# Performance work log

Hardware: AMD Instinct MI355X
Metric: run time of the kernel (lower is better)

## Reference

```python
import jax, jax.numpy as jnp
import numpy as np

S = 4096      # total packed tokens
B = 8         # number of variable-length segments
E = 1152      # embed_dim (SigLIP2 so400m)
H = 16        # num_heads
D = E // H    # head_dim = 72


def setup_inputs() -> dict:
    key = jax.random.key(0)
    ks = jax.random.split(key, 8)
    w_std = 0.02
    theta = jax.random.uniform(ks[1], (S, D), jnp.float32, 0.0, 2.0 * np.pi)
    return {
        "hidden_states": jax.random.normal(ks[0], (S, E), jnp.float32),
        "cu_seqlens": jnp.arange(B + 1, dtype=jnp.int32) * (S // B),
        "cos": jnp.cos(theta),
        "sin": jnp.sin(theta),
        "Wq": jax.random.normal(ks[2], (E, E), jnp.float32) * w_std,
        "bq": jnp.zeros((E,), jnp.float32),
        "Wk": jax.random.normal(ks[3], (E, E), jnp.float32) * w_std,
        "bk": jnp.zeros((E,), jnp.float32),
        "Wv": jax.random.normal(ks[4], (E, E), jnp.float32) * w_std,
        "bv": jnp.zeros((E,), jnp.float32),
        "Wo": jax.random.normal(ks[5], (E, E), jnp.float32) * w_std,
        "bo": jnp.zeros((E,), jnp.float32),
    }


def _rotate_half(x):
    x1, x2 = jnp.split(x, 2, axis=-1)
    return jnp.concatenate((-x2, x1), axis=-1)


def reference(hidden_states, cu_seqlens, cos, sin, Wq, bq, Wk, bk, Wv, bv, Wo, bo):
    seq_len = hidden_states.shape[0]
    scale = np.float32(D) ** -0.5
    # projections -> [S, H, D]
    q = (hidden_states @ Wq.T + bq).reshape(seq_len, H, D)
    k = (hidden_states @ Wk.T + bk).reshape(seq_len, H, D)
    v = (hidden_states @ Wv.T + bv).reshape(seq_len, H, D)
    # inline RoPE (apply_rotary_pos_emb_vision): cos/sin broadcast over heads
    c = cos[:, None, :]
    s = sin[:, None, :]
    q = q * c + _rotate_half(q) * s
    k = k * c + _rotate_half(k) * s
    # segment id per token from cu_seqlens; block-diagonal attention mask
    seg = jnp.searchsorted(cu_seqlens[1:], jnp.arange(seq_len, dtype=cu_seqlens.dtype), side="right")
    mask = seg[:, None] == seg[None, :]                     # [S, S]
    scores = jnp.einsum("shd,thd->hst", q, k) * scale       # [H, S, S]
    neg = jnp.finfo(scores.dtype).min
    scores = jnp.where(mask[None, :, :], scores, neg)
    probs = jax.nn.softmax(scores, axis=-1)
    attn = jnp.einsum("hst,thd->shd", probs, v).reshape(seq_len, E)
    return attn @ Wo.T + bo
```

## Files before the change

### kernel.cpp

```cpp
#include <hip/hip_runtime.h>
#include <float.h>

#define S_LEN 4096
#define E_DIM 1152
#define NH    16
#define HD    72
#define HD2   36
#define NQKV  3456

typedef __attribute__((ext_vector_type(4))) float f32x4;
typedef __attribute__((ext_vector_type(8))) _Float16 f16x8;

__device__ __forceinline__ unsigned short f2h(float f) {
    union { _Float16 h; unsigned short u; } c;
    c.h = (_Float16)f;
    return c.u;
}

__device__ __forceinline__ void gload_lds16(const unsigned short* g, unsigned short* l) {
    __builtin_amdgcn_global_load_lds(
        (const __attribute__((address_space(1))) unsigned int*)g,
        (__attribute__((address_space(3))) unsigned int*)l, 16, 0, 0);
}

__global__ __launch_bounds__(256)
void pack_f16(const float* __restrict__ hs, const float* __restrict__ wq,
              const float* __restrict__ wk, const float* __restrict__ wv,
              const float* __restrict__ wo,
              unsigned short* __restrict__ hs_h, unsigned short* __restrict__ wqkv_h,
              unsigned short* __restrict__ wo_h)
{
    const float* src; unsigned short* dst; int n4;
    const int WSZ = E_DIM * E_DIM;
    switch (blockIdx.z) {
        case 0: src = hs; dst = hs_h;             n4 = S_LEN * E_DIM / 4; break;
        case 1: src = wq; dst = wqkv_h;           n4 = WSZ / 4; break;
        case 2: src = wk; dst = wqkv_h + WSZ;     n4 = WSZ / 4; break;
        case 3: src = wv; dst = wqkv_h + 2 * WSZ; n4 = WSZ / 4; break;
        default: src = wo; dst = wo_h;            n4 = WSZ / 4; break;
    }
    for (int i = blockIdx.x * 256 + threadIdx.x; i < n4; i += gridDim.x * 256) {
        f32x4 x = ((const f32x4*)src)[i];
        ushort4 hv;
        hv.x = f2h(x[0]); hv.y = f2h(x[1]); hv.z = f2h(x[2]); hv.w = f2h(x[3]);
        ((ushort4*)dst)[i] = hv;
    }
}

__global__ __launch_bounds__(256, 4)
void gemm_qkv_f16(const unsigned short* __restrict__ Ah, const unsigned short* __restrict__ Wh,
                  const float* __restrict__ bq, const float* __restrict__ bk,
                  const float* __restrict__ bv,
                  float* __restrict__ oq, float* __restrict__ ok, float* __restrict__ ov)
{
    __shared__ unsigned short sA[128 * 64];
    __shared__ unsigned short sB[128 * 64];
    const int tid  = threadIdx.x;
    const int w    = tid >> 6, lane = tid & 63;
    const int quad = lane >> 4, m = lane & 15;
    const int wr   = w & 1,  wc = w >> 1;

    const int bid = blockIdx.x;
    const int lin = (bid & 7) * 108 + (bid >> 3);
    const int n_t = lin >> 5;
    const int m_t = lin & 31;
    const int m0  = m_t * 128;
    const int n0  = n_t * 128;

    const int srow = lane >> 3;
    const int skc  = (lane & 7) ^ srow;

    f32x4 acc[4][4];
    #pragma unroll
    for (int i = 0; i < 4; ++i)
        #pragma unroll
        for (int j = 0; j < 4; ++j) acc[i][j] = (f32x4){0.f, 0.f, 0.f, 0.f};

    const int rm7 = m & 7;

    for (int k0 = 0; k0 < E_DIM; k0 += 64) {
        #pragma unroll
        for (int c = 0; c < 4; ++c) {
            int r = 32 * w + 8 * c + srow;
            gload_lds16(Ah + (size_t)(m0 + r) * E_DIM + k0 + skc * 8, &sA[(32 * w + 8 * c) * 64]);
            gload_lds16(Wh + (size_t)(n0 + r) * E_DIM + k0 + skc * 8, &sB[(32 * w + 8 * c) * 64]);
        }
        __syncthreads();

        #pragma unroll
        for (int k3 = 0; k3 < 2; ++k3) {
            f16x8 ah[4], bh[4];
            #pragma unroll
            for (int t = 0; t < 4; ++t) {
                int pc = ((k3 << 2) + quad) ^ rm7;
                ah[t] = *(const f16x8*)&sA[(64 * wr + 16 * t + m) * 64 + pc * 8];
                bh[t] = *(const f16x8*)&sB[(64 * wc + 16 * t + m) * 64 + pc * 8];
            }
            #pragma unroll
            for (int rt = 0; rt < 4; ++rt)
                #pragma unroll
                for (int ct = 0; ct < 4; ++ct)
                    acc[rt][ct] = __builtin_amdgcn_mfma_f32_16x16x32_f16(ah[rt], bh[ct], acc[rt][ct], 0, 0, 0);
        }
        __syncthreads();
    }

    const int which = n0 / E_DIM;
    const int n0l = n0 - which * E_DIM;
    const float* bp = (which == 0) ? bq : (which == 1) ? bk : bv;
    float* Cp       = (which == 0) ? oq : (which == 1) ? ok : ov;
    #pragma unroll
    for (int ct = 0; ct < 4; ++ct) {
        int col = n0l + 64 * wc + 16 * ct + m;
        float bias = bp[col];
        #pragma unroll
        for (int rt = 0; rt < 4; ++rt)
            #pragma unroll
            for (int reg = 0; reg < 4; ++reg) {
                int row = m0 + 64 * wr + 16 * rt + 4 * quad + reg;
                Cp[(size_t)row * E_DIM + col] = acc[rt][ct][reg] + bias;
            }
    }
}

__global__ __launch_bounds__(256, 4)
void gemm_out_f16(const unsigned short* __restrict__ Ah, const unsigned short* __restrict__ Wh,
                  const float* __restrict__ bo, float* __restrict__ Cp)
{
    __shared__ unsigned short sA[64 * 64];
    __shared__ unsigned short sB[128 * 64];
    const int tid  = threadIdx.x;
    const int w    = tid >> 6, lane = tid & 63;
    const int quad = lane >> 4, m = lane & 15;
    const int m0   = blockIdx.y * 64;
    const int n0   = blockIdx.x * 128;

    const int srow = lane >> 3;
    const int skc  = (lane & 7) ^ srow;

    f32x4 acc[4][2];
    #pragma unroll
    for (int i = 0; i < 4; ++i)
        #pragma unroll
        for (int j = 0; j < 2; ++j) acc[i][j] = (f32x4){0.f, 0.f, 0.f, 0.f};

    const int rm7 = m & 7;

    for (int k0 = 0; k0 < E_DIM; k0 += 64) {
        #pragma unroll
        for (int c = 0; c < 2; ++c) {
            int r = 16 * w + 8 * c + srow;
            gload_lds16(Ah + (size_t)(m0 + r) * E_DIM + k0 + skc * 8, &sA[(16 * w + 8 * c) * 64]);
        }
        #pragma unroll
        for (int c = 0; c < 4; ++c) {
            int r = 32 * w + 8 * c + srow;
            gload_lds16(Wh + (size_t)(n0 + r) * E_DIM + k0 + skc * 8, &sB[(32 * w + 8 * c) * 64]);
        }
        __syncthreads();
        #pragma unroll
        for (int k3 = 0; k3 < 2; ++k3) {
            f16x8 ah[4], bh[2];
            int pc = ((k3 << 2) + quad) ^ rm7;
            #pragma unroll
            for (int t = 0; t < 4; ++t)
                ah[t] = *(const f16x8*)&sA[(16 * t + m) * 64 + pc * 8];
            #pragma unroll
            for (int ct = 0; ct < 2; ++ct)
                bh[ct] = *(const f16x8*)&sB[(32 * w + 16 * ct + m) * 64 + pc * 8];
            #pragma unroll
            for (int rt = 0; rt < 4; ++rt)
                #pragma unroll
                for (int ct = 0; ct < 2; ++ct)
                    acc[rt][ct] = __builtin_amdgcn_mfma_f32_16x16x32_f16(ah[rt], bh[ct], acc[rt][ct], 0, 0, 0);
        }
        __syncthreads();
    }

    #pragma unroll
    for (int ct = 0; ct < 2; ++ct) {
        int col = n0 + 32 * w + 16 * ct + m;
        float bias = bo[col];
        #pragma unroll
        for (int rt = 0; rt < 4; ++rt)
            #pragma unroll
            for (int reg = 0; reg < 4; ++reg) {
                int row = m0 + 16 * rt + 4 * quad + reg;
                Cp[(size_t)row * E_DIM + col] = acc[rt][ct][reg] + bias;
            }
    }
}

__global__ __launch_bounds__(256)
void vtrans(const float* __restrict__ v, unsigned short* __restrict__ vt)
{
    __shared__ unsigned short tile[HD][72];
    const int h = blockIdx.y;
    const int s0 = blockIdx.x * 64;
    for (int task = threadIdx.x; task < 64 * 18; task += 256) {
        int r = task / 18, c = task % 18;
        f32x4 x = *(const f32x4*)(v + (size_t)(s0 + r) * E_DIM + h * HD + (c << 2));
        tile[(c << 2) + 0][r] = f2h(x[0]);
        tile[(c << 2) + 1][r] = f2h(x[1]);
        tile[(c << 2) + 2][r] = f2h(x[2]);
        tile[(c << 2) + 3][r] = f2h(x[3]);
    }
    __syncthreads();
    for (int task = threadIdx.x; task < HD * 8; task += 256) {
        int d = task / 8, cc = task % 8;
        uint4 val = *(const uint4*)&tile[d][cc << 3];
        *(uint4*)(vt + ((size_t)h * HD + d) * S_LEN + s0 + (cc << 3)) = val;
    }
}

__global__ __launch_bounds__(256, 4)
void attn_rope(const float* __restrict__ qf, const float* __restrict__ kf,
               const float* __restrict__ cosb, const float* __restrict__ sinb,
               const unsigned short* __restrict__ vt, const int* __restrict__ cu,
               int nseg, unsigned short* __restrict__ out)
{
    __shared__ unsigned short ks_s[64][72];
    __shared__ unsigned short vs_s[80][72];
    __shared__ unsigned short ss_s[64][72];

    const int tid  = threadIdx.x;
    const int w    = tid >> 6;
    const int lane = tid & 63;
    const int quad = lane >> 4;
    const int m    = lane & 15;
    const int h    = blockIdx.y;
    const int qb0  = blockIdx.x * 64;
    const float scale = 0.11785113019775793f;

    {
        uint4 zz = make_uint4(0u, 0u, 0u, 0u);
        if (tid < 72) {
            int r = 72 + tid / 9, c = tid % 9;
            *(uint4*)&vs_s[r][c << 3] = zz;
        }
    }

    int rs_r[4], re_r[4];
    #pragma unroll
    for (int reg = 0; reg < 4; ++reg) {
        int row = qb0 + 16 * w + 4 * quad + reg;
        int st = 0;
        for (int i = 1; i < nseg; ++i) if (cu[i] <= row) st = i;
        rs_r[reg] = cu[st];
        re_r[reg] = cu[st + 1];
    }
    int st0 = 0, st1 = 0;
    for (int i = 1; i < nseg; ++i) {
        if (cu[i] <= qb0) st0 = i;
        if (cu[i] <= qb0 + 63) st1 = i;
    }
    const int kstart = cu[st0];
    const int kend   = cu[st1 + 1];

    for (int task = tid; task < 64 * 9; task += 256) {
        int row = task / 9, d0 = (task % 9) << 2;
        int s = qb0 + row;
        const float* xr = qf + (size_t)s * E_DIM + h * HD;
        f32x4 a  = *(const f32x4*)(xr + d0);
        f32x4 b  = *(const f32x4*)(xr + d0 + HD2);
        f32x4 c1 = *(const f32x4*)(cosb + (size_t)s * HD + d0);
        f32x4 s1 = *(const f32x4*)(sinb + (size_t)s * HD + d0);
        f32x4 c2 = *(const f32x4*)(cosb + (size_t)s * HD + d0 + HD2);
        f32x4 s2 = *(const f32x4*)(sinb + (size_t)s * HD + d0 + HD2);
        f32x4 r1 = a * c1 - b * s1;
        f32x4 r2 = b * c2 + a * s2;
        uint2 u1, u2;
        u1.x = (unsigned)f2h(r1[0]) | ((unsigned)f2h(r1[1]) << 16);
        u1.y = (unsigned)f2h(r1[2]) | ((unsigned)f2h(r1[3]) << 16);
        u2.x = (unsigned)f2h(r2[0]) | ((unsigned)f2h(r2[1]) << 16);
        u2.y = (unsigned)f2h(r2[2]) | ((unsigned)f2h(r2[3]) << 16);
        *(uint2*)&ks_s[row][d0]       = u1;
        *(uint2*)&ks_s[row][d0 + HD2] = u2;
    }
    __syncthreads();

    f16x8 qfr[3];
    {
        const unsigned short* qrow = &ks_s[16 * w + m][0];
        #pragma unroll
        for (int k3 = 0; k3 < 3; ++k3) {
            bool pad = (k3 == 2) && (quad != 0);
            int off = pad ? 0 : (k3 * 32 + quad * 8);
            f16x8 val = *(const f16x8*)(qrow + off);
            f16x8 z = {0, 0, 0, 0, 0, 0, 0, 0};
            qfr[k3] = pad ? z : val;
        }
    }

    f32x4 acc_o[5];
    #pragma unroll
    for (int i = 0; i < 5; ++i) acc_o[i] = (f32x4){0.f, 0.f, 0.f, 0.f};
    float l_r[4] = {0.f, 0.f, 0.f, 0.f};

    for (int kb_i = kstart; kb_i < kend; kb_i += 64) {
        __syncthreads();
        for (int task = tid; task < 64 * 9; task += 256) {
            int row = task / 9, d0 = (task % 9) << 2;
            int s = kb_i + row; if (s >= kend) s = kend - 1;
            const float* xr = kf + (size_t)s * E_DIM + h * HD;
            f32x4 a  = *(const f32x4*)(xr + d0);
            f32x4 b  = *(const f32x4*)(xr + d0 + HD2);
            f32x4 c1 = *(const f32x4*)(cosb + (size_t)s * HD + d0);
            f32x4 s1 = *(const f32x4*)(sinb + (size_t)s * HD + d0);
            f32x4 c2 = *(const f32x4*)(cosb + (size_t)s * HD + d0 + HD2);
            f32x4 s2 = *(const f32x4*)(sinb + (size_t)s * HD + d0 + HD2);
            f32x4 r1 = a * c1 - b * s1;
            f32x4 r2 = b * c2 + a * s2;
            uint2 u1, u2;
            u1.x = (unsigned)f2h(r1[0]) | ((unsigned)f2h(r1[1]) << 16);
            u1.y = (unsigned)f2h(r1[2]) | ((unsigned)f2h(r1[3]) << 16);
            u2.x = (unsigned)f2h(r2[0]) | ((unsigned)f2h(r2[1]) << 16);
            u2.y = (unsigned)f2h(r2[2]) | ((unsigned)f2h(r2[3]) << 16);
            *(uint2*)&ks_s[row][d0]       = u1;
            *(uint2*)&ks_s[row][d0 + HD2] = u2;
        }
        for (int slot = tid; slot < 72 * 8; slot += 256) {
            int d = slot / 8, c = slot % 8;
            int kk0 = kb_i + (c << 3);
            if (kk0 > S_LEN - 8) kk0 = S_LEN - 8;
            uint4 val = *(const uint4*)(vt + ((size_t)h * HD + d) * S_LEN + kk0);
            *(uint4*)&vs_s[d][c << 3] = val;
        }
        __syncthreads();

        f32x4 sacc[4];
        #pragma unroll
        for (int ct = 0; ct < 4; ++ct) sacc[ct] = (f32x4){0.f, 0.f, 0.f, 0.f};
        #pragma unroll
        for (int ct = 0; ct < 4; ++ct) {
            const unsigned short* krow = &ks_s[16 * ct + m][0];
            #pragma unroll
            for (int k3 = 0; k3 < 3; ++k3) {
                bool pad = (k3 == 2) && (quad != 0);
                int off = pad ? 0 : (k3 * 32 + quad * 8);
                f16x8 bfr = *(const f16x8*)(krow + off);
                f16x8 z = {0, 0, 0, 0, 0, 0, 0, 0};
                bfr = pad ? z : bfr;
                sacc[ct] = __builtin_amdgcn_mfma_f32_16x16x32_f16(qfr[k3], bfr, sacc[ct], 0, 0, 0);
            }
        }

        #pragma unroll
        for (int ct = 0; ct < 4; ++ct) {
            int key = kb_i + 16 * ct + m;
            #pragma unroll
            for (int reg = 0; reg < 4; ++reg) {
                bool valid = (key >= rs_r[reg]) && (key < re_r[reg]);
                float p = valid ? __expf(sacc[ct][reg] * scale) : 0.f;
                l_r[reg] += p;
                ss_s[16 * w + 4 * quad + reg][16 * ct + m] = f2h(p);
            }
        }

        {
            const unsigned short* prow = &ss_s[16 * w + m][0];
            f16x8 pf0 = *(const f16x8*)(prow + quad * 8);
            f16x8 pf1 = *(const f16x8*)(prow + 32 + quad * 8);
            #pragma unroll
            for (int ct2 = 0; ct2 < 5; ++ct2) {
                const unsigned short* vrow = &vs_s[16 * ct2 + m][0];
                f16x8 vf0 = *(const f16x8*)(vrow + quad * 8);
                f16x8 vf1 = *(const f16x8*)(vrow + 32 + quad * 8);
                acc_o[ct2] = __builtin_amdgcn_mfma_f32_16x16x32_f16(pf0, vf0, acc_o[ct2], 0, 0, 0);
                acc_o[ct2] = __builtin_amdgcn_mfma_f32_16x16x32_f16(pf1, vf1, acc_o[ct2], 0, 0, 0);
            }
        }
    }

    #pragma unroll
    for (int reg = 0; reg < 4; ++reg) {
        float l = l_r[reg];
        l += __shfl_xor(l, 1);
        l += __shfl_xor(l, 2);
        l += __shfl_xor(l, 4);
        l += __shfl_xor(l, 8);
        l_r[reg] = l;
    }

    #pragma unroll
    for (int reg = 0; reg < 4; ++reg) {
        float linv = (l_r[reg] > 0.f) ? 1.f / l_r[reg] : 0.f;
        int row = qb0 + 16 * w + 4 * quad + reg;
        unsigned short* orow = out + (size_t)row * E_DIM + h * HD;
        #pragma unroll
        for (int ct2 = 0; ct2 < 5; ++ct2) {
            int col = 16 * ct2 + m;
            if (col < HD) orow[col] = f2h(acc_o[ct2][reg] * linv);
        }
    }
}

extern "C" void kernel_launch(void* const* d_in, const int* in_sizes, int n_in,
                              void* d_out, int out_size, void* d_ws, size_t ws_size,
                              hipStream_t stream)
{
    const float* hs   = (const float*)d_in[0];
    const int*   cu   = (const int*)d_in[1];
    const float* cosb = (const float*)d_in[2];
    const float* sinb = (const float*)d_in[3];
    const float* Wq   = (const float*)d_in[4];
    const float* bq   = (const float*)d_in[5];
    const float* Wk   = (const float*)d_in[6];
    const float* bk   = (const float*)d_in[7];
    const float* Wv   = (const float*)d_in[8];
    const float* bv   = (const float*)d_in[9];
    const float* Wo   = (const float*)d_in[10];
    const float* bo   = (const float*)d_in[11];
    float* outp = (float*)d_out;

    const size_t mat = (size_t)S_LEN * E_DIM;
    float* qf = (float*)d_ws;
    float* kf = qf + mat;
    float* vf = kf + mat;
    unsigned short* hs_h   = (unsigned short*)(vf + mat);
    unsigned short* wqkv_h = hs_h + mat;
    unsigned short* wo_h   = wqkv_h + (size_t)NQKV * E_DIM;
    unsigned short* vtb    = wo_h + (size_t)E_DIM * E_DIM;
    unsigned short* attn_h = hs_h;

    const int nseg = in_sizes[1] - 1;

    dim3 gpack(512, 1, 5);
    pack_f16<<<gpack, 256, 0, stream>>>(hs, Wq, Wk, Wv, Wo, hs_h, wqkv_h, wo_h);

    gemm_qkv_f16<<<dim3(864), 256, 0, stream>>>(hs_h, wqkv_h, bq, bk, bv, qf, kf, vf);

    dim3 gvt(S_LEN / 64, NH, 1);
    vtrans<<<gvt, 256, 0, stream>>>(vf, vtb);

    dim3 gattn(S_LEN / 64, NH, 1);
    attn_rope<<<gattn, 256, 0, stream>>>(qf, kf, cosb, sinb, vtb, cu, nseg, attn_h);

    dim3 gout(E_DIM / 128, S_LEN / 64, 1);
    gemm_out_f16<<<gout, 256, 0, stream>>>(attn_h, wo_h, bo, outp);
}
```

Measured before the change: 224.3 us.

## Precompute RoPE'd fp16 Q/K and pass attention probabilities via register shuffles

RoPE and the fp16 conversion of Q and K move out of the attention loop into a pre-pass kernel that also transposes V. This stops each query block from recomputing RoPE on every K tile. The attention kernel now loads head-major fp16 K directly and computes S^T so the probabilities can be rearranged into the P·V operand with lane shuffles instead of an LDS round-trip. Packed conversion intrinsics replace scalar f16 conversions. The cost is extra global traffic for the fp16 Q/K buffers and one more read pass over q/k in the pre-pass kernel.

```diff
diff --git a/kernel.cpp b/kernel.cpp
--- a/kernel.cpp
+++ b/kernel.cpp
@@ -9,11 +9,17 @@
 #define NQKV  3456
 
 typedef __attribute__((ext_vector_type(4))) float f32x4;
+typedef __attribute__((ext_vector_type(2))) __fp16 fp16v2;
 typedef __attribute__((ext_vector_type(8))) _Float16 f16x8;
 
 __device__ __forceinline__ unsigned short f2h(float f) {
     union { _Float16 h; unsigned short u; } c;
     c.h = (_Float16)f;
+    return c.u;
+}
+__device__ __forceinline__ unsigned pack2h(float a, float b) {
+    union { fp16v2 v; unsigned u; } c;
+    c.v = __builtin_amdgcn_cvt_pkrtz(a, b);
     return c.u;
 }
 
@@ -41,9 +47,10 @@
     }
     for (int i = blockIdx.x * 256 + threadIdx.x; i < n4; i += gridDim.x * 256) {
         f32x4 x = ((const f32x4*)src)[i];
-        ushort4 hv;
-        hv.x = f2h(x[0]); hv.y = f2h(x[1]); hv.z = f2h(x[2]); hv.w = f2h(x[3]);
-        ((ushort4*)dst)[i] = hv;
+        uint2 hv;
+        hv.x = pack2h(x[0], x[1]);
+        hv.y = pack2h(x[2], x[3]);
+        ((uint2*)dst)[i] = hv;
     }
 }
 
@@ -192,36 +199,64 @@
 }
 
 __global__ __launch_bounds__(256)
-void vtrans(const float* __restrict__ v, unsigned short* __restrict__ vt)
+void rope_v_pack(const float* __restrict__ qf, const float* __restrict__ kf,
+                 const float* __restrict__ vf,
+                 const float* __restrict__ cosb, const float* __restrict__ sinb,
+                 unsigned short* __restrict__ qb, unsigned short* __restrict__ kb,
+                 unsigned short* __restrict__ vt)
 {
     __shared__ unsigned short tile[HD][72];
-    const int h = blockIdx.y;
+    const int h  = blockIdx.y;
     const int s0 = blockIdx.x * 64;
-    for (int task = threadIdx.x; task < 64 * 18; task += 256) {
-        int r = task / 18, c = task % 18;
-        f32x4 x = *(const f32x4*)(v + (size_t)(s0 + r) * E_DIM + h * HD + (c << 2));
-        tile[(c << 2) + 0][r] = f2h(x[0]);
-        tile[(c << 2) + 1][r] = f2h(x[1]);
-        tile[(c << 2) + 2][r] = f2h(x[2]);
-        tile[(c << 2) + 3][r] = f2h(x[3]);
-    }
-    __syncthreads();
-    for (int task = threadIdx.x; task < HD * 8; task += 256) {
-        int d = task / 8, cc = task % 8;
-        uint4 val = *(const uint4*)&tile[d][cc << 3];
-        *(uint4*)(vt + ((size_t)h * HD + d) * S_LEN + s0 + (cc << 3)) = val;
+    const int z  = blockIdx.z;
+    if (z < 2) {
+        const float* x = (z == 0) ? qf : kf;
+        unsigned short* ob = (z == 0) ? qb : kb;
+        for (int task = threadIdx.x; task < 64 * 9; task += 256) {
+            int sl = task / 9, c = task % 9;
+            int s = s0 + sl;
+            int d0 = c << 2;
+            const float* xr = x + (size_t)s * E_DIM + h * HD;
+            f32x4 a  = *(const f32x4*)(xr + d0);
+            f32x4 b  = *(const f32x4*)(xr + d0 + HD2);
+            f32x4 c1 = *(const f32x4*)(cosb + (size_t)s * HD + d0);
+            f32x4 s1 = *(const f32x4*)(sinb + (size_t)s * HD + d0);
+            f32x4 c2 = *(const f32x4*)(cosb + (size_t)s * HD + d0 + HD2);
+            f32x4 s2 = *(const f32x4*)(sinb + (size_t)s * HD + d0 + HD2);
+            f32x4 r1 = a * c1 - b * s1;
+            f32x4 r2 = b * c2 + a * s2;
+            unsigned short* orow = ob + ((size_t)h * S_LEN + s) * HD;
+            uint2 u1, u2;
+            u1.x = pack2h(r1[0], r1[1]); u1.y = pack2h(r1[2], r1[3]);
+            u2.x = pack2h(r2[0], r2[1]); u2.y = pack2h(r2[2], r2[3]);
+            *(uint2*)(orow + d0)       = u1;
+            *(uint2*)(orow + d0 + HD2) = u2;
+        }
+    } else {
+        for (int task = threadIdx.x; task < 64 * 18; task += 256) {
+            int r = task / 18, c = task % 18;
+            f32x4 x = *(const f32x4*)(vf + (size_t)(s0 + r) * E_DIM + h * HD + (c << 2));
+            tile[(c << 2) + 0][r] = f2h(x[0]);
+            tile[(c << 2) + 1][r] = f2h(x[1]);
+            tile[(c << 2) + 2][r] = f2h(x[2]);
+            tile[(c << 2) + 3][r] = f2h(x[3]);
+        }
+        __syncthreads();
+        for (int task = threadIdx.x; task < HD * 8; task += 256) {
+            int d = task / 8, cc = task % 8;
+            uint4 val = *(const uint4*)&tile[d][cc << 3];
+            *(uint4*)(vt + ((size_t)h * HD + d) * S_LEN + s0 + (cc << 3)) = val;
+        }
     }
 }
 
 __global__ __launch_bounds__(256, 4)
-void attn_rope(const float* __restrict__ qf, const float* __restrict__ kf,
-               const float* __restrict__ cosb, const float* __restrict__ sinb,
-               const unsigned short* __restrict__ vt, const int* __restrict__ cu,
-               int nseg, unsigned short* __restrict__ out)
+void attn_f16(const unsigned short* __restrict__ qb, const unsigned short* __restrict__ kb,
+              const unsigned short* __restrict__ vt, const int* __restrict__ cu,
+              int nseg, unsigned short* __restrict__ out)
 {
     __shared__ unsigned short ks_s[64][72];
     __shared__ unsigned short vs_s[80][72];
-    __shared__ unsigned short ss_s[64][72];
 
     const int tid  = threadIdx.x;
     const int w    = tid >> 6;
@@ -240,15 +275,11 @@
         }
     }
 
-    int rs_r[4], re_r[4];
-    #pragma unroll
-    for (int reg = 0; reg < 4; ++reg) {
-        int row = qb0 + 16 * w + 4 * quad + reg;
-        int st = 0;
-        for (int i = 1; i < nseg; ++i) if (cu[i] <= row) st = i;
-        rs_r[reg] = cu[st];
-        re_r[reg] = cu[st + 1];
-    }
+    const int qrow = qb0 + 16 * w + m;
+    int st = 0;
+    for (int i = 1; i < nseg; ++i) if (cu[i] <= qrow) st = i;
+    const int rs = cu[st], re = cu[st + 1];
+
     int st0 = 0, st1 = 0;
     for (int i = 1; i < nseg; ++i) {
         if (cu[i] <= qb0) st0 = i;
@@ -257,36 +288,14 @@
     const int kstart = cu[st0];
     const int kend   = cu[st1 + 1];
 
-    for (int task = tid; task < 64 * 9; task += 256) {
-        int row = task / 9, d0 = (task % 9) << 2;
-        int s = qb0 + row;
-        const float* xr = qf + (size_t)s * E_DIM + h * HD;
-        f32x4 a  = *(const f32x4*)(xr + d0);
-        f32x4 b  = *(const f32x4*)(xr + d0 + HD2);
-        f32x4 c1 = *(const f32x4*)(cosb + (size_t)s * HD + d0);
-        f32x4 s1 = *(const f32x4*)(sinb + (size_t)s * HD + d0);
-        f32x4 c2 = *(const f32x4*)(cosb + (size_t)s * HD + d0 + HD2);
-        f32x4 s2 = *(const f32x4*)(sinb + (size_t)s * HD + d0 + HD2);
-        f32x4 r1 = a * c1 - b * s1;
-        f32x4 r2 = b * c2 + a * s2;
-        uint2 u1, u2;
-        u1.x = (unsigned)f2h(r1[0]) | ((unsigned)f2h(r1[1]) << 16);
-        u1.y = (unsigned)f2h(r1[2]) | ((unsigned)f2h(r1[3]) << 16);
-        u2.x = (unsigned)f2h(r2[0]) | ((unsigned)f2h(r2[1]) << 16);
-        u2.y = (unsigned)f2h(r2[2]) | ((unsigned)f2h(r2[3]) << 16);
-        *(uint2*)&ks_s[row][d0]       = u1;
-        *(uint2*)&ks_s[row][d0 + HD2] = u2;
-    }
-    __syncthreads();
-
     f16x8 qfr[3];
     {
-        const unsigned short* qrow = &ks_s[16 * w + m][0];
+        const unsigned short* qrp = qb + ((size_t)h * S_LEN + qrow) * HD;
         #pragma unroll
         for (int k3 = 0; k3 < 3; ++k3) {
             bool pad = (k3 == 2) && (quad != 0);
             int off = pad ? 0 : (k3 * 32 + quad * 8);
-            f16x8 val = *(const f16x8*)(qrow + off);
+            f16x8 val = *(const f16x8*)(qrp + off);
             f16x8 z = {0, 0, 0, 0, 0, 0, 0, 0};
             qfr[k3] = pad ? z : val;
         }
@@ -295,29 +304,18 @@
     f32x4 acc_o[5];
     #pragma unroll
     for (int i = 0; i < 5; ++i) acc_o[i] = (f32x4){0.f, 0.f, 0.f, 0.f};
-    float l_r[4] = {0.f, 0.f, 0.f, 0.f};
+    float l_s = 0.f;
+
+    const int srcA = 32 * (quad & 1) + m;
+    const bool sel = (quad >> 1) != 0;
 
     for (int kb_i = kstart; kb_i < kend; kb_i += 64) {
         __syncthreads();
-        for (int task = tid; task < 64 * 9; task += 256) {
-            int row = task / 9, d0 = (task % 9) << 2;
-            int s = kb_i + row; if (s >= kend) s = kend - 1;
-            const float* xr = kf + (size_t)s * E_DIM + h * HD;
-            f32x4 a  = *(const f32x4*)(xr + d0);
-            f32x4 b  = *(const f32x4*)(xr + d0 + HD2);
-            f32x4 c1 = *(const f32x4*)(cosb + (size_t)s * HD + d0);
-            f32x4 s1 = *(const f32x4*)(sinb + (size_t)s * HD + d0);
-            f32x4 c2 = *(const f32x4*)(cosb + (size_t)s * HD + d0 + HD2);
-            f32x4 s2 = *(const f32x4*)(sinb + (size_t)s * HD + d0 + HD2);
-            f32x4 r1 = a * c1 - b * s1;
-            f32x4 r2 = b * c2 + a * s2;
-            uint2 u1, u2;
-            u1.x = (unsigned)f2h(r1[0]) | ((unsigned)f2h(r1[1]) << 16);
-            u1.y = (unsigned)f2h(r1[2]) | ((unsigned)f2h(r1[3]) << 16);
-            u2.x = (unsigned)f2h(r2[0]) | ((unsigned)f2h(r2[1]) << 16);
-            u2.y = (unsigned)f2h(r2[2]) | ((unsigned)f2h(r2[3]) << 16);
-            *(uint2*)&ks_s[row][d0]       = u1;
-            *(uint2*)&ks_s[row][d0 + HD2] = u2;
+        for (int slot = tid; slot < 64 * 9; slot += 256) {
+            int r = slot / 9, c = slot % 9;
+            int krow = kb_i + r; if (krow >= kend) krow = kend - 1;
+            uint4 val = *(const uint4*)(kb + ((size_t)h * S_LEN + krow) * HD + (c << 3));
+            *(uint4*)&ks_s[r][c << 3] = val;
         }
         for (int slot = tid; slot < 72 * 8; slot += 256) {
             int d = slot / 8, c = slot % 8;
@@ -338,53 +336,61 @@
             for (int k3 = 0; k3 < 3; ++k3) {
                 bool pad = (k3 == 2) && (quad != 0);
                 int off = pad ? 0 : (k3 * 32 + quad * 8);
-                f16x8 bfr = *(const f16x8*)(krow + off);
+                f16x8 kfr = *(const f16x8*)(krow + off);
                 f16x8 z = {0, 0, 0, 0, 0, 0, 0, 0};
-                bfr = pad ? z : bfr;
-                sacc[ct] = __builtin_amdgcn_mfma_f32_16x16x32_f16(qfr[k3], bfr, sacc[ct], 0, 0, 0);
-            }
-        }
-
+                kfr = pad ? z : kfr;
+                sacc[ct] = __builtin_amdgcn_mfma_f32_16x16x32_f16(kfr, qfr[k3], sacc[ct], 0, 0, 0);
+            }
+        }
+
+        unsigned pk[4][2];
         #pragma unroll
         for (int ct = 0; ct < 4; ++ct) {
-            int key = kb_i + 16 * ct + m;
+            float p[4];
             #pragma unroll
             for (int reg = 0; reg < 4; ++reg) {
-                bool valid = (key >= rs_r[reg]) && (key < re_r[reg]);
-                float p = valid ? __expf(sacc[ct][reg] * scale) : 0.f;
-                l_r[reg] += p;
-                ss_s[16 * w + 4 * quad + reg][16 * ct + m] = f2h(p);
-            }
-        }
-
-        {
-            const unsigned short* prow = &ss_s[16 * w + m][0];
-            f16x8 pf0 = *(const f16x8*)(prow + quad * 8);
-            f16x8 pf1 = *(const f16x8*)(prow + 32 + quad * 8);
-            #pragma unroll
-            for (int ct2 = 0; ct2 < 5; ++ct2) {
-                const unsigned short* vrow = &vs_s[16 * ct2 + m][0];
-                f16x8 vf0 = *(const f16x8*)(vrow + quad * 8);
-                f16x8 vf1 = *(const f16x8*)(vrow + 32 + quad * 8);
-                acc_o[ct2] = __builtin_amdgcn_mfma_f32_16x16x32_f16(pf0, vf0, acc_o[ct2], 0, 0, 0);
-                acc_o[ct2] = __builtin_amdgcn_mfma_f32_16x16x32_f16(pf1, vf1, acc_o[ct2], 0, 0, 0);
-            }
-        }
-    }
+                int key = kb_i + 16 * ct + 4 * quad + reg;
+                bool valid = (key >= rs) && (key < re);
+                p[reg] = valid ? __expf(sacc[ct][reg] * scale) : 0.f;
+                l_s += p[reg];
+            }
+            pk[ct][0] = pack2h(p[0], p[1]);
+            pk[ct][1] = pack2h(p[2], p[3]);
+        }
+
+        f16x8 pf[2];
+        #pragma unroll
+        for (int c = 0; c < 2; ++c) {
+            union { unsigned d[4]; f16x8 v; } fb;
+            #pragma unroll
+            for (int r = 0; r < 2; ++r) {
+                int x0 = __shfl((int)pk[2 * c][r],     srcA);
+                int x1 = __shfl((int)pk[2 * c + 1][r], srcA);
+                fb.d[r] = (unsigned)(sel ? x1 : x0);
+                int y0 = __shfl((int)pk[2 * c][r],     srcA + 16);
+                int y1 = __shfl((int)pk[2 * c + 1][r], srcA + 16);
+                fb.d[2 + r] = (unsigned)(sel ? y1 : y0);
+            }
+            pf[c] = fb.v;
+        }
+
+        #pragma unroll
+        for (int ct2 = 0; ct2 < 5; ++ct2) {
+            const unsigned short* vrow = &vs_s[16 * ct2 + m][0];
+            f16x8 vf0 = *(const f16x8*)(vrow + quad * 8);
+            f16x8 vf1 = *(const f16x8*)(vrow + 32 + quad * 8);
+            acc_o[ct2] = __builtin_amdgcn_mfma_f32_16x16x32_f16(pf[0], vf0, acc_o[ct2], 0, 0, 0);
+            acc_o[ct2] = __builtin_amdgcn_mfma_f32_16x16x32_f16(pf[1], vf1, acc_o[ct2], 0, 0, 0);
+        }
+    }
+
+    l_s += __shfl_xor(l_s, 16);
+    l_s += __shfl_xor(l_s, 32);
 
     #pragma unroll
     for (int reg = 0; reg < 4; ++reg) {
-        float l = l_r[reg];
-        l += __shfl_xor(l, 1);
-        l += __shfl_xor(l, 2);
-        l += __shfl_xor(l, 4);
-        l += __shfl_xor(l, 8);
-        l_r[reg] = l;
-    }
-
-    #pragma unroll
-    for (int reg = 0; reg < 4; ++reg) {
-        float linv = (l_r[reg] > 0.f) ? 1.f / l_r[reg] : 0.f;
+        float lr = __shfl(l_s, 4 * quad + reg);
+        float linv = (lr > 0.f) ? 1.f / lr : 0.f;
         int row = qb0 + 16 * w + 4 * quad + reg;
         unsigned short* orow = out + (size_t)row * E_DIM + h * HD;
         #pragma unroll
@@ -421,7 +427,9 @@
     unsigned short* wqkv_h = hs_h + mat;
     unsigned short* wo_h   = wqkv_h + (size_t)NQKV * E_DIM;
     unsigned short* vtb    = wo_h + (size_t)E_DIM * E_DIM;
-    unsigned short* attn_h = hs_h;
+    unsigned short* kbb    = vtb + mat;
+    unsigned short* qbb    = hs_h;
+    unsigned short* attn_h = (unsigned short*)qf;
 
     const int nseg = in_sizes[1] - 1;
 
@@ -430,11 +438,11 @@
 
     gemm_qkv_f16<<<dim3(864), 256, 0, stream>>>(hs_h, wqkv_h, bq, bk, bv, qf, kf, vf);
 
-    dim3 gvt(S_LEN / 64, NH, 1);
-    vtrans<<<gvt, 256, 0, stream>>>(vf, vtb);
+    dim3 grv(S_LEN / 64, NH, 3);
+    rope_v_pack<<<grv, 256, 0, stream>>>(qf, kf, vf, cosb, sinb, qbb, kbb, vtb);
 
     dim3 gattn(S_LEN / 64, NH, 1);
-    attn_rope<<<gattn, 256, 0, stream>>>(qf, kf, cosb, sinb, vtb, cu, nseg, attn_h);
+    attn_f16<<<gattn, 256, 0, stream>>>(qbb, kbb, vtb, cu, nseg, attn_h);
 
     dim3 gout(E_DIM / 128, S_LEN / 64, 1);
     gemm_out_f16<<<gout, 256, 0, stream>>>(attn_h, wo_h, bo, outp);
```

Result: no change. 228.1 us (+1.7%).
